# Kernel tuning notes

Hardware: AMD Instinct MI355X
Metric: run time of the kernel (lower is better)

The kernel has to match this reference:

```python
import jax, jax.numpy as jnp
import numpy as np

N_NODES = 50000
N_REL = 8
N_EDGES = 100000
IN_SIZE = 128
OUT_SIZE = 128


def setup_inputs() -> dict:
    key = jax.random.key(0)
    k1, k2, k3, k4, k5 = jax.random.split(key, 5)
    inp = jax.random.normal(k1, (N_NODES, IN_SIZE), dtype=jnp.float32)
    src = jax.random.randint(k2, (N_REL, N_EDGES), 0, N_NODES, dtype=jnp.int32)
    dst = jax.random.randint(k3, (N_REL, N_EDGES), 0, N_NODES, dtype=jnp.int32)
    vals = jax.random.uniform(k4, (N_REL, N_EDGES), dtype=jnp.float32)
    weights = jax.random.normal(k5, (N_REL, IN_SIZE, OUT_SIZE), dtype=jnp.float32) * (1.0 / np.sqrt(IN_SIZE))
    return {"inp": inp, "src": src, "dst": dst, "vals": vals, "weights": weights}


def reference(inp, src, dst, vals, weights):
    # Per-relation sparse adj @ inp:  agg[r] = A_r @ inp, A_r given as COO edges.
    n_nodes = inp.shape[0]

    def rel_agg(s, d, v):
        msgs = v[:, None] * inp[s]                      # [E, in]
        return jax.ops.segment_sum(msgs, d, num_segments=n_nodes)  # [N, in]

    agg = jax.vmap(rel_agg)(src, dst, vals)             # [R, N, in]
    # concat along features then block-stacked weight matmul == per-relation
    # matmul summed over relations: out = sum_r agg[r] @ W[r]
    out = jnp.einsum('rni,rio->no', agg, weights)       # [N, out]
    return out
```

## Files before the change

kernel.cpp:

```cpp
#include <hip/hip_runtime.h>


constexpr int IN  = 128;
constexpr int OUT = 128;
constexpr int LDK = 136;

typedef __attribute__((ext_vector_type(8))) short bf16x8;
typedef __attribute__((ext_vector_type(4))) float f32x4;

__device__ inline unsigned short f2bf(float f) {
    unsigned int u = __float_as_uint(f);
    u += 0x7fffu + ((u >> 16) & 1u);
    return (unsigned short)(u >> 16);
}
__device__ inline float bflo(unsigned int u) { return __uint_as_float(u << 16); }
__device__ inline float bfhi(unsigned int u) { return __uint_as_float(u & 0xffff0000u); }

__global__ __launch_bounds__(256) void conv_inp_kernel(
    const float* __restrict__ x, unsigned short* __restrict__ y, int n8)
{
    const int i = blockIdx.x * 256 + threadIdx.x;
    if (i >= n8) return;
    const float4 a = ((const float4*)x)[i * 2];
    const float4 b = ((const float4*)x)[i * 2 + 1];
    uint4 o;
    o.x = (unsigned)f2bf(a.x) | ((unsigned)f2bf(a.y) << 16);
    o.y = (unsigned)f2bf(a.z) | ((unsigned)f2bf(a.w) << 16);
    o.z = (unsigned)f2bf(b.x) | ((unsigned)f2bf(b.y) << 16);
    o.w = (unsigned)f2bf(b.z) | ((unsigned)f2bf(b.w) << 16);
    ((uint4*)y)[i] = o;
}

__global__ __launch_bounds__(256) void conv_w_kernel(
    const float* __restrict__ w, unsigned short* __restrict__ wt, int total)
{
    const int t = blockIdx.x * 256 + threadIdx.x;
    if (t >= total) return;
    const int r = t >> 14, rem = t & 16383;
    const int n = rem >> 7, k = rem & 127;
    wt[t] = f2bf(w[(r << 14) + (k << 7) + n]);
}

__global__ __launch_bounds__(256) void mfma_gemm(
    const unsigned short* __restrict__ inpb,
    const unsigned short* __restrict__ wt,
    unsigned short* __restrict__ h, int rel_base, int n_nodes)
{
    __shared__ unsigned short As[128 * LDK];

    const int rel = rel_base + blockIdx.y;
    const int row0 = blockIdx.x * 128;
    const int tid = threadIdx.x;
    const int wave = tid >> 6, lane = tid & 63;
    const int m = lane & 15, q = lane >> 4;

    {
        const int r = tid >> 1;
        const int half = (tid & 1) * 64;
        const int grow = row0 + r;
        const uint4* gp = (const uint4*)(inpb + (size_t)grow * IN + half);
        uint4* lp = (uint4*)&As[r * LDK + half];
        #pragma unroll
        for (int i = 0; i < 8; ++i) {
            uint4 v = make_uint4(0u, 0u, 0u, 0u);
            if (grow < n_nodes) v = gp[i];
            lp[i] = v;
        }
    }

    bf16x8 bfrag[2][4];
    {
        const unsigned short* wtr = wt + ((size_t)rel * OUT + wave * 32) * IN;
        #pragma unroll
        for (int nt = 0; nt < 2; ++nt)
            #pragma unroll
            for (int ks = 0; ks < 4; ++ks)
                bfrag[nt][ks] = *(const bf16x8*)(
                    wtr + (size_t)(nt * 16 + m) * IN + ks * 32 + q * 8);
    }

    __syncthreads();

    f32x4 acc[8][2];
    #pragma unroll
    for (int mt = 0; mt < 8; ++mt)
        #pragma unroll
        for (int nt = 0; nt < 2; ++nt)
            acc[mt][nt] = (f32x4){0.f, 0.f, 0.f, 0.f};

    #pragma unroll
    for (int ks = 0; ks < 4; ++ks) {
        bf16x8 a[8];
        #pragma unroll
        for (int mt = 0; mt < 8; ++mt)
            a[mt] = *(const bf16x8*)&As[(mt * 16 + m) * LDK + ks * 32 + q * 8];
        #pragma unroll
        for (int mt = 0; mt < 8; ++mt) {
            acc[mt][0] = __builtin_amdgcn_mfma_f32_16x16x32_bf16(
                a[mt], bfrag[0][ks], acc[mt][0], 0, 0, 0);
            acc[mt][1] = __builtin_amdgcn_mfma_f32_16x16x32_bf16(
                a[mt], bfrag[1][ks], acc[mt][1], 0, 0, 0);
        }
    }

    unsigned short* hrel = h + (size_t)blockIdx.y * n_nodes * OUT;
    #pragma unroll
    for (int mt = 0; mt < 8; ++mt) {
        #pragma unroll
        for (int rg = 0; rg < 4; ++rg) {
            const int row = row0 + mt * 16 + q * 4 + rg;
            if (row < n_nodes) {
                unsigned short* hp = hrel + (size_t)row * OUT + wave * 32 + m;
                hp[0]  = f2bf(acc[mt][0][rg]);
                hp[16] = f2bf(acc[mt][1][rg]);
            }
        }
    }
}

__global__ __launch_bounds__(256) void fill_kernel(
    const int* __restrict__ src, const int* __restrict__ dst,
    const float* __restrict__ vals, int* __restrict__ counts,
    int2* __restrict__ bucket, int4* __restrict__ spill,
    int* __restrict__ spill_cnt, int n_edges, int n_nodes,
    int cap, int spill_max)
{
    const int e = blockIdx.x * 256 + threadIdx.x;
    if (e >= n_edges) return;
    const size_t g = (size_t)blockIdx.y * n_edges + e;
    const int d = dst[g];
    const int enc = blockIdx.y * n_nodes + src[g];
    const int pos = atomicAdd(&counts[d], 1);
    if (pos < cap) {
        bucket[(size_t)d * cap + pos] = make_int2(enc, __float_as_int(vals[g]));
    } else {
        const int sp = atomicAdd(spill_cnt, 1);
        if (sp < spill_max)
            spill[sp] = make_int4(d, enc, __float_as_int(vals[g]), 0);
    }
}

__global__ __launch_bounds__(256) void gather_kernel(
    const unsigned short* __restrict__ h, const int2* __restrict__ bucket,
    const int* __restrict__ counts, float* __restrict__ out,
    int n_nodes, int cap, int accum)
{
    const int node = blockIdx.x * 8 + (threadIdx.x >> 5);
    const int lane = threadIdx.x & 31;
    if (node >= n_nodes) return;
    int cnt = counts[node];
    if (cnt > cap) cnt = cap;
    const int2* __restrict__ b = bucket + (size_t)node * cap;
    float4* __restrict__ op = (float4*)(out + (size_t)node * OUT);

    float4 acc = accum ? op[lane] : make_float4(0.f, 0.f, 0.f, 0.f);
    int j = 0;
    for (; j + 4 <= cnt; j += 4) {
        const int2 r0 = b[j], r1 = b[j + 1], r2 = b[j + 2], r3 = b[j + 3];
        const uint2 h0 = ((const uint2*)(h + (size_t)r0.x * OUT))[lane];
        const uint2 h1 = ((const uint2*)(h + (size_t)r1.x * OUT))[lane];
        const uint2 h2 = ((const uint2*)(h + (size_t)r2.x * OUT))[lane];
        const uint2 h3 = ((const uint2*)(h + (size_t)r3.x * OUT))[lane];
        const float v0 = __int_as_float(r0.y), v1 = __int_as_float(r1.y);
        const float v2 = __int_as_float(r2.y), v3 = __int_as_float(r3.y);
        acc.x += v0*bflo(h0.x) + v1*bflo(h1.x) + v2*bflo(h2.x) + v3*bflo(h3.x);
        acc.y += v0*bfhi(h0.x) + v1*bfhi(h1.x) + v2*bfhi(h2.x) + v3*bfhi(h3.x);
        acc.z += v0*bflo(h0.y) + v1*bflo(h1.y) + v2*bflo(h2.y) + v3*bflo(h3.y);
        acc.w += v0*bfhi(h0.y) + v1*bfhi(h1.y) + v2*bfhi(h2.y) + v3*bfhi(h3.y);
    }
    for (; j < cnt; ++j) {
        const int2 r0 = b[j];
        const float v = __int_as_float(r0.y);
        const uint2 hv = ((const uint2*)(h + (size_t)r0.x * OUT))[lane];
        acc.x += v * bflo(hv.x); acc.y += v * bfhi(hv.x);
        acc.z += v * bflo(hv.y); acc.w += v * bfhi(hv.y);
    }
    op[lane] = acc;
}

__global__ __launch_bounds__(256) void spill_kernel(
    const unsigned short* __restrict__ h, const int4* __restrict__ spill,
    const int* __restrict__ spill_cnt, float* __restrict__ out, int spill_max)
{
    int n = *spill_cnt;
    if (n > spill_max) n = spill_max;
    const int w = (blockIdx.x * 256 + threadIdx.x) >> 6;
    const int lane = threadIdx.x & 63;
    const int nw = gridDim.x * 4;
    for (int i = w; i < n; i += nw) {
        const int4 s = spill[i];
        const float v = __int_as_float(s.z);
        const unsigned int u = ((const unsigned int*)(h + (size_t)s.y * OUT))[lane];
        float* __restrict__ orow = out + (size_t)s.x * OUT;
        __hip_atomic_fetch_add(orow + lane * 2,     v * bflo(u),
                               __ATOMIC_RELAXED, __HIP_MEMORY_SCOPE_AGENT);
        __hip_atomic_fetch_add(orow + lane * 2 + 1, v * bfhi(u),
                               __ATOMIC_RELAXED, __HIP_MEMORY_SCOPE_AGENT);
    }
}

__global__ __launch_bounds__(256) void scatter_kernel(
    const unsigned short* __restrict__ h, const int* __restrict__ src,
    const int* __restrict__ dst, const float* __restrict__ vals,
    float* __restrict__ out, int n_edges)
{
    const int e = blockIdx.x * 8 + (threadIdx.x >> 5);
    if (e >= n_edges) return;
    const int lane = threadIdx.x & 31;
    const int s = src[e];
    const int d = dst[e];
    const float v = vals[e];
    const unsigned int* __restrict__ hrow =
        (const unsigned int*)(h + (size_t)s * OUT);
    float* __restrict__ orow = out + (size_t)d * OUT;
    #pragma unroll
    for (int kk = 0; kk < 2; ++kk) {
        const int jj = lane + kk * 32;
        const unsigned int u = hrow[jj];
        __hip_atomic_fetch_add(orow + jj * 2,     v * bflo(u),
                               __ATOMIC_RELAXED, __HIP_MEMORY_SCOPE_AGENT);
        __hip_atomic_fetch_add(orow + jj * 2 + 1, v * bfhi(u),
                               __ATOMIC_RELAXED, __HIP_MEMORY_SCOPE_AGENT);
    }
}

extern "C" void kernel_launch(void* const* d_in, const int* in_sizes, int n_in,
                              void* d_out, int out_size, void* d_ws, size_t ws_size,
                              hipStream_t stream) {
    const float* inp     = (const float*)d_in[0];
    const int*   src     = (const int*)  d_in[1];
    const int*   dst     = (const int*)  d_in[2];
    const float* vals    = (const float*)d_in[3];
    const float* weights = (const float*)d_in[4];
    float* out = (float*)d_out;

    const int n_nodes = in_sizes[0] / IN;
    const int n_rel   = in_sizes[4] / (IN * OUT);
    const int n_edges = in_sizes[1] / n_rel;

    auto align_up = [](size_t x) { return (x + 255) & ~(size_t)255; };
    const int SPILL_MAX = 65536;
    const size_t sz_inpb   = align_up((size_t)n_nodes * IN * 2);
    const size_t sz_wt     = align_up((size_t)n_rel * IN * OUT * 2);
    const size_t sz_counts = align_up((size_t)(n_nodes + 1) * 4);
    const size_t sz_spill  = align_up((size_t)SPILL_MAX * 16);
    const size_t fixed = sz_inpb + sz_wt + sz_counts + sz_spill;

    const int conv_n8 = n_nodes * IN / 8;
    const int wt_tot  = n_rel * IN * OUT;
    const int gemm_gx = (n_nodes + 127) / 128;
    const int gath_gx = (n_nodes + 7) / 8;
    const int fill_gx = (n_edges + 255) / 256;

    {
        const size_t sz_h = (size_t)n_rel * n_nodes * OUT * 2;
        int cap = 0;
        const int caps[] = {64, 48, 32, 24, 20};
        for (int c : caps) {
            if (fixed + sz_h + align_up((size_t)n_nodes * c * 8) <= ws_size) {
                cap = c; break;
            }
        }
        if (cap > 0) {
            char* p = (char*)d_ws;
            unsigned short* inpb = (unsigned short*)p;  p += sz_inpb;
            unsigned short* wtb  = (unsigned short*)p;  p += sz_wt;
            int*   counts = (int*)p;    p += sz_counts;
            int4*  spill  = (int4*)p;   p += sz_spill;
            unsigned short* h = (unsigned short*)p;     p += sz_h;
            int2*  bucket = (int2*)p;
            int*   spill_cnt = counts + n_nodes;

            conv_inp_kernel<<<(conv_n8 + 255) / 256, 256, 0, stream>>>(
                inp, inpb, conv_n8);
            conv_w_kernel<<<(wt_tot + 255) / 256, 256, 0, stream>>>(
                weights, wtb, wt_tot);
            hipMemsetAsync(counts, 0, (size_t)(n_nodes + 1) * 4, stream);
            dim3 fg(fill_gx, n_rel);
            fill_kernel<<<fg, 256, 0, stream>>>(src, dst, vals, counts, bucket,
                                                spill, spill_cnt, n_edges,
                                                n_nodes, cap, SPILL_MAX);
            dim3 gg(gemm_gx, n_rel);
            mfma_gemm<<<gg, 256, 0, stream>>>(inpb, wtb, h, 0, n_nodes);
            gather_kernel<<<gath_gx, 256, 0, stream>>>(h, bucket, counts, out,
                                                       n_nodes, cap, 0);
            spill_kernel<<<128, 256, 0, stream>>>(h, spill, spill_cnt, out,
                                                  SPILL_MAX);
            return;
        }
    }

    {
        const size_t sz_h = (size_t)n_nodes * OUT * 2;
        int cap = 0;
        const int caps[] = {16, 12, 8};
        for (int c : caps) {
            if (fixed + sz_h + align_up((size_t)n_nodes * c * 8) <= ws_size) {
                cap = c; break;
            }
        }
        if (cap > 0) {
            char* p = (char*)d_ws;
            unsigned short* inpb = (unsigned short*)p;  p += sz_inpb;
            unsigned short* wtb  = (unsigned short*)p;  p += sz_wt;
            int*   counts = (int*)p;    p += sz_counts;
            int4*  spill  = (int4*)p;   p += sz_spill;
            unsigned short* h = (unsigned short*)p;     p += sz_h;
            int2*  bucket = (int2*)p;
            int*   spill_cnt = counts + n_nodes;

            conv_inp_kernel<<<(conv_n8 + 255) / 256, 256, 0, stream>>>(
                inp, inpb, conv_n8);
            conv_w_kernel<<<(wt_tot + 255) / 256, 256, 0, stream>>>(
                weights, wtb, wt_tot);
            for (int r = 0; r < n_rel; ++r) {
                const size_t eoff = (size_t)r * n_edges;
                hipMemsetAsync(counts, 0, (size_t)(n_nodes + 1) * 4, stream);
                dim3 fg(fill_gx, 1);
                fill_kernel<<<fg, 256, 0, stream>>>(src + eoff, dst + eoff,
                                                    vals + eoff, counts, bucket,
                                                    spill, spill_cnt, n_edges,
                                                    n_nodes, cap, SPILL_MAX);
                dim3 gg(gemm_gx, 1);
                mfma_gemm<<<gg, 256, 0, stream>>>(inpb, wtb, h, r, n_nodes);
                gather_kernel<<<gath_gx, 256, 0, stream>>>(h, bucket, counts,
                                                           out, n_nodes, cap,
                                                           r > 0 ? 1 : 0);
                spill_kernel<<<128, 256, 0, stream>>>(h, spill, spill_cnt, out,
                                                      SPILL_MAX);
            }
            return;
        }
    }

    {
        char* p = (char*)d_ws;
        unsigned short* inpb = (unsigned short*)p;  p += sz_inpb;
        unsigned short* wtb  = (unsigned short*)p;  p += sz_wt;
        unsigned short* h = (unsigned short*)p;

        conv_inp_kernel<<<(conv_n8 + 255) / 256, 256, 0, stream>>>(
            inp, inpb, conv_n8);
        conv_w_kernel<<<(wt_tot + 255) / 256, 256, 0, stream>>>(
            weights, wtb, wt_tot);
        hipMemsetAsync(out, 0, (size_t)n_nodes * OUT * 4, stream);
        const int sgx = (n_edges + 7) / 8;
        for (int r = 0; r < n_rel; ++r) {
            const size_t eoff = (size_t)r * n_edges;
            dim3 gg(gemm_gx, 1);
            mfma_gemm<<<gg, 256, 0, stream>>>(inpb, wtb, h, r, n_nodes);
            scatter_kernel<<<sgx, 256, 0, stream>>>(h, src + eoff, dst + eoff,
                                                    vals + eoff, out, n_edges);
        }
    }
}
```

Before: 222.2 us.

## Bin edges per 64-node tile per XCD and aggregate in shared memory

Adds a path that buckets edges by 64-node destination bins, with separate cells per XCD read from the hardware register, so atomic counters stay local to each XCD's cache. A new aggregation kernel accumulates each bin's messages in a 32KB LDS tile using shared atomics and then writes the output rows once. The goal is to replace the per-node bucket fill and gather with coarser bins that need fewer global atomics and give better write locality. The cost is LDS atomic contention, a large per-block LDS footprint that limits occupancy, and binned storage of 8 XCDs x bins x 256 entries.

Result: slower. 866.2 us (+289.8%).

```diff
diff --git a/kernel.cpp b/kernel.cpp
--- a/kernel.cpp
+++ b/kernel.cpp
@@ -4,6 +4,8 @@
 constexpr int IN  = 128;
 constexpr int OUT = 128;
 constexpr int LDK = 136;
+constexpr int NPB = 64;
+constexpr int NXCD = 8;
 
 typedef __attribute__((ext_vector_type(8))) short bf16x8;
 typedef __attribute__((ext_vector_type(4))) float f32x4;
@@ -115,6 +117,104 @@
                 hp[16] = f2bf(acc[mt][1][rg]);
             }
         }
+    }
+}
+
+__global__ __launch_bounds__(256) void bin_fill_kernel(
+    const int* __restrict__ src, const int* __restrict__ dst,
+    const float* __restrict__ vals, int* __restrict__ bin_cnt,
+    int2* __restrict__ binned, int4* __restrict__ spill,
+    int* __restrict__ spill_cnt, int n_edges, int n_nodes,
+    int nbins, int cap, int spill_max)
+{
+    int xcd;
+    asm volatile("s_getreg_b32 %0, hwreg(HW_REG_XCC_ID)" : "=s"(xcd));
+    xcd &= (NXCD - 1);
+    const int e = blockIdx.x * 256 + threadIdx.x;
+    if (e >= n_edges) return;
+    const size_t g = (size_t)blockIdx.y * n_edges + e;
+    const int d = dst[g];
+    const int enc = blockIdx.y * n_nodes + src[g];
+    const int bin = d >> 6;
+    const int packed = ((d & 63) << 19) | enc;
+    const int cell = xcd * nbins + bin;
+    const int pos = atomicAdd(&bin_cnt[cell], 1);
+    if (pos < cap) {
+        binned[(size_t)cell * cap + pos] =
+            make_int2(packed, __float_as_int(vals[g]));
+    } else {
+        const int sp = atomicAdd(spill_cnt, 1);
+        if (sp < spill_max)
+            spill[sp] = make_int4(d, enc, __float_as_int(vals[g]), 0);
+    }
+}
+
+__global__ __launch_bounds__(256) void bin_agg_kernel(
+    const unsigned short* __restrict__ h, const int2* __restrict__ binned,
+    const int* __restrict__ bin_cnt, float* __restrict__ out,
+    int n_nodes, int nbins, int cap)
+{
+    __shared__ float accum[NPB * OUT];
+    const int bin = blockIdx.x;
+    const int tid = threadIdx.x;
+    #pragma unroll
+    for (int i = 0; i < NPB * OUT / 256; ++i)
+        accum[i * 256 + tid] = 0.f;
+    __syncthreads();
+
+    const int wave = tid >> 6, lane = tid & 63;
+    const unsigned int* __restrict__ hw = (const unsigned int*)h;
+
+    for (int xc = 0; xc < NXCD; ++xc) {
+        const int cell = xc * nbins + bin;
+        int cnt = bin_cnt[cell];
+        if (cnt > cap) cnt = cap;
+        const int2* __restrict__ b = binned + (size_t)cell * cap;
+        for (int base = wave * 4; base < cnt; base += 16) {
+            if (base + 4 <= cnt) {
+                const int2 r0 = b[base],     r1 = b[base + 1];
+                const int2 r2 = b[base + 2], r3 = b[base + 3];
+                const unsigned int h0 = hw[(size_t)(r0.x & 0x7ffff) * 64 + lane];
+                const unsigned int h1 = hw[(size_t)(r1.x & 0x7ffff) * 64 + lane];
+                const unsigned int h2 = hw[(size_t)(r2.x & 0x7ffff) * 64 + lane];
+                const unsigned int h3 = hw[(size_t)(r3.x & 0x7ffff) * 64 + lane];
+                const float v0 = __int_as_float(r0.y), v1 = __int_as_float(r1.y);
+                const float v2 = __int_as_float(r2.y), v3 = __int_as_float(r3.y);
+                float* a0 = &accum[((r0.x >> 19) & 63) * OUT + 2 * lane];
+                float* a1 = &accum[((r1.x >> 19) & 63) * OUT + 2 * lane];
+                float* a2 = &accum[((r2.x >> 19) & 63) * OUT + 2 * lane];
+                float* a3 = &accum[((r3.x >> 19) & 63) * OUT + 2 * lane];
+                atomicAdd(a0,     v0 * bflo(h0));
+                atomicAdd(a0 + 1, v0 * bfhi(h0));
+                atomicAdd(a1,     v1 * bflo(h1));
+                atomicAdd(a1 + 1, v1 * bfhi(h1));
+                atomicAdd(a2,     v2 * bflo(h2));
+                atomicAdd(a2 + 1, v2 * bfhi(h2));
+                atomicAdd(a3,     v3 * bflo(h3));
+                atomicAdd(a3 + 1, v3 * bfhi(h3));
+            } else {
+                for (int k = base; k < cnt; ++k) {
+                    const int2 r0 = b[k];
+                    const unsigned int h0 =
+                        hw[(size_t)(r0.x & 0x7ffff) * 64 + lane];
+                    const float v0 = __int_as_float(r0.y);
+                    float* a0 = &accum[((r0.x >> 19) & 63) * OUT + 2 * lane];
+                    atomicAdd(a0,     v0 * bflo(h0));
+                    atomicAdd(a0 + 1, v0 * bfhi(h0));
+                }
+            }
+        }
+    }
+    __syncthreads();
+
+    const int n = tid >> 2, qd = tid & 3;
+    const int node = bin * NPB + n;
+    if (node < n_nodes) {
+        float4* __restrict__ op = (float4*)(out + (size_t)node * OUT);
+        const float4* ap = (const float4*)&accum[n * OUT];
+        #pragma unroll
+        for (int i = 0; i < 8; ++i)
+            op[i * 4 + qd] = ap[i * 4 + qd];
     }
 }
 
@@ -242,15 +342,59 @@
     const int SPILL_MAX = 65536;
     const size_t sz_inpb   = align_up((size_t)n_nodes * IN * 2);
     const size_t sz_wt     = align_up((size_t)n_rel * IN * OUT * 2);
-    const size_t sz_counts = align_up((size_t)(n_nodes + 1) * 4);
     const size_t sz_spill  = align_up((size_t)SPILL_MAX * 16);
-    const size_t fixed = sz_inpb + sz_wt + sz_counts + sz_spill;
 
     const int conv_n8 = n_nodes * IN / 8;
     const int wt_tot  = n_rel * IN * OUT;
     const int gemm_gx = (n_nodes + 127) / 128;
     const int gath_gx = (n_nodes + 7) / 8;
     const int fill_gx = (n_edges + 255) / 256;
+    const int nbins   = (n_nodes + NPB - 1) / NPB;
+
+    if ((size_t)n_rel * n_nodes < (1u << 19)) {
+        const size_t sz_h    = (size_t)n_rel * n_nodes * OUT * 2;
+        const size_t sz_bcnt = align_up((size_t)(NXCD * nbins + 1) * 4);
+        int cap = 0;
+        const int caps[] = {256, 192};
+        for (int c : caps) {
+            const size_t sz_binned =
+                align_up((size_t)NXCD * nbins * c * 8);
+            if (sz_inpb + sz_wt + sz_bcnt + sz_spill + sz_h + sz_binned
+                <= ws_size) { cap = c; break; }
+        }
+        if (cap > 0) {
+            const size_t sz_binned = align_up((size_t)NXCD * nbins * cap * 8);
+            char* p = (char*)d_ws;
+            unsigned short* inpb = (unsigned short*)p;  p += sz_inpb;
+            unsigned short* wtb  = (unsigned short*)p;  p += sz_wt;
+            int*   bin_cnt = (int*)p;   p += sz_bcnt;
+            int4*  spill   = (int4*)p;  p += sz_spill;
+            unsigned short* h = (unsigned short*)p;     p += sz_h;
+            int2*  binned  = (int2*)p;  p += sz_binned;
+            int*   spill_cnt = bin_cnt + NXCD * nbins;
+
+            conv_inp_kernel<<<(conv_n8 + 255) / 256, 256, 0, stream>>>(
+                inp, inpb, conv_n8);
+            conv_w_kernel<<<(wt_tot + 255) / 256, 256, 0, stream>>>(
+                weights, wtb, wt_tot);
+            hipMemsetAsync(bin_cnt, 0, (size_t)(NXCD * nbins + 1) * 4, stream);
+            dim3 fg(fill_gx, n_rel);
+            bin_fill_kernel<<<fg, 256, 0, stream>>>(src, dst, vals, bin_cnt,
+                                                    binned, spill, spill_cnt,
+                                                    n_edges, n_nodes, nbins,
+                                                    cap, SPILL_MAX);
+            dim3 gg(gemm_gx, n_rel);
+            mfma_gemm<<<gg, 256, 0, stream>>>(inpb, wtb, h, 0, n_nodes);
+            bin_agg_kernel<<<nbins, 256, 0, stream>>>(h, binned, bin_cnt, out,
+                                                      n_nodes, nbins, cap);
+            spill_kernel<<<128, 256, 0, stream>>>(h, spill, spill_cnt, out,
+                                                  SPILL_MAX);
+            return;
+        }
+    }
+
+    const size_t sz_counts = align_up((size_t)(n_nodes + 1) * 4);
+    const size_t fixed = sz_inpb + sz_wt + sz_counts + sz_spill;
 
     {
         const size_t sz_h = (size_t)n_rel * n_nodes * OUT * 2;
```
